# Optimization experiments

Measured on AMD Instinct MI355X. Metric: run time of the kernel, lower is better.

Reference implementation:

```python
import jax, jax.numpy as jnp
import numpy as np

VOCAB, EMB_DIM, HIDDEN, NUM_CLASSES = 100000, 128, 256, 20
B, S = 4096, 200


def setup_inputs() -> dict:
    key = jax.random.key(0)
    k1, k2, k3, k4, k5, k6, k7 = jax.random.split(key, 7)
    x = jax.random.randint(k1, (B, S), 0, VOCAB, dtype=jnp.int64)
    seq_lengths = jnp.maximum(jax.random.randint(k2, (B,), 0, S, dtype=jnp.int64), 1)
    emb = jax.random.normal(k3, (VOCAB, EMB_DIM), dtype=jnp.float32) * 0.02
    emb = emb.at[0].set(0.0)  # padding_idx=0
    W1 = jax.random.normal(k4, (EMB_DIM, HIDDEN), dtype=jnp.float32) * (1.0 / np.sqrt(EMB_DIM))
    b1 = jax.random.normal(k5, (HIDDEN,), dtype=jnp.float32) * 0.01
    W2 = jax.random.normal(k6, (HIDDEN, NUM_CLASSES), dtype=jnp.float32) * (1.0 / np.sqrt(HIDDEN))
    b2 = jax.random.normal(k7, (NUM_CLASSES,), dtype=jnp.float32) * 0.01
    return {"x": x, "seq_lengths": seq_lengths, "emb": emb, "W1": W1, "b1": b1, "W2": W2, "b2": b2}


def reference(x, seq_lengths, emb, W1, b1, W2, b2):
    # Embedding lookup: [B, S, D]
    e = emb[x]
    # Masked mean over first seq_lengths[i] positions (fused, no per-sample loop)
    mask = (jnp.arange(S)[None, :] < seq_lengths[:, None]).astype(e.dtype)  # [B, S]
    pooled = jnp.einsum('bsd,bs->bd', e, mask) / seq_lengths[:, None].astype(e.dtype)
    # MLP (dropout is identity in eval mode)
    hidden = jax.nn.relu(pooled @ W1 + b1)
    return hidden @ W2 + b2
```

## Files before the change

### kernel.cpp

```cpp
#include <hip/hip_runtime.h>
#include <hip/hip_bf16.h>

#define B 4096
#define S 200
#define EMB_DIM 128
#define HIDDEN 256
#define NUM_CLASSES 20
#define VOCAB 100000
#define NSLICE 8
#define SDIM 16
#define SP 224

typedef __attribute__((ext_vector_type(8))) unsigned short ushort8;

__device__ __forceinline__ unsigned short f2bf(float f) {
    unsigned u = __float_as_uint(f);
    unsigned r = u + 0x7fffu + ((u >> 16) & 1u);
    return (unsigned short)(r >> 16);
}

__global__ __launch_bounds__(256) void convert_kernel(
    const float* __restrict__ emb,
    unsigned short* __restrict__ embh)
{
    const int t = threadIdx.x;
    const int v = blockIdx.x * 16 + (t >> 4);
    const int d = t & 15;
    const float4 a = *(const float4*)(emb + (long)v * EMB_DIM + d * 8);
    const float4 b = *(const float4*)(emb + (long)v * EMB_DIM + d * 8 + 4);
    ushort8 o;
    o[0] = f2bf(a.x); o[1] = f2bf(a.y); o[2] = f2bf(a.z); o[3] = f2bf(a.w);
    o[4] = f2bf(b.x); o[5] = f2bf(b.y); o[6] = f2bf(b.z); o[7] = f2bf(b.w);
    const int s = d >> 1, h = d & 1;
    *(ushort8*)(embh + (long)s * VOCAB * SDIM + (long)v * SDIM + h * 8) = o;
}

__global__ __launch_bounds__(256) void gather_kernel(
    const int* __restrict__ x,
    const int* __restrict__ lens,
    const unsigned short* __restrict__ embh,
    float* __restrict__ pooled)
{
    __shared__ int sidx[8][SP];
    __shared__ int sL[8];

    const int t  = threadIdx.x;
    const int s  = blockIdx.x & 7;
    const int rg = blockIdx.x >> 3;
    const unsigned short* embS = embh + (long)s * VOCAB * SDIM;

    {
        const int r   = t >> 5;
        const int p0  = t & 31;
        const int row = rg * 8 + r;
        const int L   = lens[row];
        if (p0 == 0) sL[r] = L;
        for (int p = p0; p < SP; p += 32)
            sidx[r][p] = (p < L) ? x[(long)row * S + p] : 0;
    }
    __syncthreads();

    const int w  = t >> 6;
    const int l  = t & 63;
    const int pl = l >> 1;
    const int h  = l & 1;

    #pragma unroll
    for (int rr = 0; rr < 2; ++rr) {
        const int r2 = 2 * w + rr;
        const int L2 = sL[r2];
        const int nR = (L2 + 31) >> 5;

        float acc[8];
        #pragma unroll
        for (int f = 0; f < 8; ++f) acc[f] = 0.f;

        int cur = sidx[r2][pl];
        for (int it = 0; it < nR; ++it) {
            const uint4 q = *(const uint4*)(embS + (long)cur * SDIM + h * 8);
            const int nxt = (it + 1 < nR) ? sidx[r2][pl + ((it + 1) << 5)] : 0;
            acc[0] += __uint_as_float(q.x << 16);
            acc[1] += __uint_as_float(q.x & 0xffff0000u);
            acc[2] += __uint_as_float(q.y << 16);
            acc[3] += __uint_as_float(q.y & 0xffff0000u);
            acc[4] += __uint_as_float(q.z << 16);
            acc[5] += __uint_as_float(q.z & 0xffff0000u);
            acc[6] += __uint_as_float(q.w << 16);
            acc[7] += __uint_as_float(q.w & 0xffff0000u);
            cur = nxt;
        }

        #pragma unroll
        for (int st = 2; st <= 32; st <<= 1) {
            #pragma unroll
            for (int f = 0; f < 8; ++f) acc[f] += __shfl_xor(acc[f], st, 64);
        }

        if (l < 2) {
            const float invL = 1.0f / (float)L2;
            float* dst = pooled + (long)(rg * 8 + r2) * EMB_DIM + s * SDIM + h * 8;
            *(float4*)dst       = make_float4(acc[0] * invL, acc[1] * invL,
                                              acc[2] * invL, acc[3] * invL);
            *(float4*)(dst + 4) = make_float4(acc[4] * invL, acc[5] * invL,
                                              acc[6] * invL, acc[7] * invL);
        }
    }
}

#define TB 8
__global__ __launch_bounds__(256) void mlp_kernel(
    const float* __restrict__ pooled,
    const float* __restrict__ W1,
    const float* __restrict__ b1,
    const float* __restrict__ W2,
    const float* __restrict__ b2,
    float* __restrict__ out)
{
    __shared__ float P[TB][EMB_DIM];
    __shared__ float H[TB][HIDDEN];

    const int t = threadIdx.x;
    const int b0 = blockIdx.x * TB;

    for (int i = t; i < TB * EMB_DIM; i += 256)
        P[i >> 7][i & 127] = pooled[(long)b0 * EMB_DIM + i];
    __syncthreads();

    float acc[TB];
    #pragma unroll
    for (int r = 0; r < TB; ++r) acc[r] = 0.f;

    for (int k4 = 0; k4 < EMB_DIM; k4 += 4) {
        float4 p[TB];
        #pragma unroll
        for (int r = 0; r < TB; ++r) p[r] = *(const float4*)&P[r][k4];
        #pragma unroll
        for (int kk = 0; kk < 4; ++kk) {
            const float w = W1[(k4 + kk) * HIDDEN + t];
            #pragma unroll
            for (int r = 0; r < TB; ++r) {
                const float pv = (kk == 0) ? p[r].x : (kk == 1) ? p[r].y
                               : (kk == 2) ? p[r].z : p[r].w;
                acc[r] += pv * w;
            }
        }
    }

    const float bb = b1[t];
    #pragma unroll
    for (int r = 0; r < TB; ++r) H[r][t] = fmaxf(acc[r] + bb, 0.f);
    __syncthreads();

    if (t < TB * NUM_CLASSES) {
        const int r = t / NUM_CLASSES;
        const int c = t - r * NUM_CLASSES;
        float a0 = 0.f, a1 = 0.f;
        for (int k = 0; k < HIDDEN; k += 2) {
            a0 += H[r][k]     * W2[(k)     * NUM_CLASSES + c];
            a1 += H[r][k + 1] * W2[(k + 1) * NUM_CLASSES + c];
        }
        out[(long)(b0 + r) * NUM_CLASSES + c] = a0 + a1 + b2[c];
    }
}

extern "C" void kernel_launch(void* const* d_in, const int* in_sizes, int n_in,
                              void* d_out, int out_size, void* d_ws, size_t ws_size,
                              hipStream_t stream) {
    const int*   x    = (const int*)d_in[0];
    const int*   lens = (const int*)d_in[1];
    const float* emb  = (const float*)d_in[2];
    const float* W1   = (const float*)d_in[3];
    const float* b1   = (const float*)d_in[4];
    const float* W2   = (const float*)d_in[5];
    const float* b2   = (const float*)d_in[6];
    float*       out  = (float*)d_out;

    unsigned short* embh  = (unsigned short*)d_ws;
    float* pooled = (float*)((char*)d_ws + (long)VOCAB * EMB_DIM * 2);

    convert_kernel<<<VOCAB / 16, 256, 0, stream>>>(emb, embh);
    gather_kernel<<<(B / 8) * NSLICE, 256, 0, stream>>>(x, lens, embh, pooled);
    mlp_kernel<<<B / TB, 256, 0, stream>>>(pooled, W1, b1, W2, b2, out);
}
```

Before: 137.5 us.

## Partition gather by vocabulary range with per-slice partial sums

Splits the embedding-bag gather across blocks by vocabulary range instead of by embedding-dimension slice. Each block keeps a compacted shared-memory list of the tokens that fall in its vocab slice and reads full contiguous 256-byte bf16 rows. It writes per-slice partial means, which the MLP kernel then sums. The bf16 table reverts to a plain row-major layout. The aim is to keep each block's working set to one vocab slice of the table while getting contiguous row reads. The cost is an 8x larger intermediate buffer written and re-read, shared-memory atomics, padding of each list to a multiple of 16, and uneven per-slice token counts.

```diff
diff --git a/kernel.cpp b/kernel.cpp
--- a/kernel.cpp
+++ b/kernel.cpp
@@ -8,8 +8,9 @@
 #define NUM_CLASSES 20
 #define VOCAB 100000
 #define NSLICE 8
-#define SDIM 16
-#define SP 224
+#define VSLICE (VOCAB / NSLICE)
+#define RPB 8
+#define LCAP 208
 
 typedef __attribute__((ext_vector_type(8))) unsigned short ushort8;
 
@@ -23,82 +24,107 @@
     const float* __restrict__ emb,
     unsigned short* __restrict__ embh)
 {
-    const int t = threadIdx.x;
-    const int v = blockIdx.x * 16 + (t >> 4);
-    const int d = t & 15;
-    const float4 a = *(const float4*)(emb + (long)v * EMB_DIM + d * 8);
-    const float4 b = *(const float4*)(emb + (long)v * EMB_DIM + d * 8 + 4);
+    const long i = ((long)blockIdx.x * 256 + threadIdx.x) * 8;
+    const float4 a = *(const float4*)(emb + i);
+    const float4 b = *(const float4*)(emb + i + 4);
     ushort8 o;
     o[0] = f2bf(a.x); o[1] = f2bf(a.y); o[2] = f2bf(a.z); o[3] = f2bf(a.w);
     o[4] = f2bf(b.x); o[5] = f2bf(b.y); o[6] = f2bf(b.z); o[7] = f2bf(b.w);
-    const int s = d >> 1, h = d & 1;
-    *(ushort8*)(embh + (long)s * VOCAB * SDIM + (long)v * SDIM + h * 8) = o;
+    *(ushort8*)(embh + i) = o;
 }
 
 __global__ __launch_bounds__(256) void gather_kernel(
     const int* __restrict__ x,
     const int* __restrict__ lens,
     const unsigned short* __restrict__ embh,
-    float* __restrict__ pooled)
+    float* __restrict__ partial)
 {
-    __shared__ int sidx[8][SP];
-    __shared__ int sL[8];
-
-    const int t  = threadIdx.x;
-    const int s  = blockIdx.x & 7;
-    const int rg = blockIdx.x >> 3;
-    const unsigned short* embS = embh + (long)s * VOCAB * SDIM;
+    __shared__ int list[RPB][LCAP];
+    __shared__ int cnt[RPB];
+    __shared__ int pcnt[RPB];
+    __shared__ int sL[RPB];
+
+    const int t     = threadIdx.x;
+    const int slice = blockIdx.x & 7;
+    const int rg    = blockIdx.x >> 3;
+    const int vlo   = slice * VSLICE;
+
+    if (t < RPB) { cnt[t] = 0; sL[t] = lens[rg * RPB + t]; }
+    __syncthreads();
 
     {
         const int r   = t >> 5;
-        const int p0  = t & 31;
-        const int row = rg * 8 + r;
-        const int L   = lens[row];
-        if (p0 == 0) sL[r] = L;
-        for (int p = p0; p < SP; p += 32)
-            sidx[r][p] = (p < L) ? x[(long)row * S + p] : 0;
-    }
-    __syncthreads();
-
-    const int w  = t >> 6;
-    const int l  = t & 63;
-    const int pl = l >> 1;
-    const int h  = l & 1;
+        const int q   = t & 31;
+        const int row = rg * RPB + r;
+        const int L   = sL[r];
+        #pragma unroll
+        for (int j = 0; j < 7; ++j) {
+            const int p = q + 32 * j;
+            if (p < L) {
+                const int v = x[(long)row * S + p];
+                if ((unsigned)(v - vlo) < (unsigned)VSLICE) {
+                    const int pos = atomicAdd(&cnt[r], 1);
+                    if (pos < LCAP) list[r][pos] = v;
+                }
+            }
+        }
+    }
+    __syncthreads();
+
+    if (t < RPB) {
+        const int c  = cnt[t];
+        const int cp = (c + 15) & ~15;
+        for (int i = c; i < cp; ++i) list[t][i] = 0;
+        pcnt[t] = cp;
+    }
+    __syncthreads();
+
+    const int w = t >> 6;
+    const int l = t & 63;
+    const int g = l >> 4;
+    const int d = l & 15;
 
     #pragma unroll
     for (int rr = 0; rr < 2; ++rr) {
         const int r2 = 2 * w + rr;
-        const int L2 = sL[r2];
-        const int nR = (L2 + 31) >> 5;
+        const int n  = pcnt[r2];
 
         float acc[8];
         #pragma unroll
         for (int f = 0; f < 8; ++f) acc[f] = 0.f;
 
-        int cur = sidx[r2][pl];
-        for (int it = 0; it < nR; ++it) {
-            const uint4 q = *(const uint4*)(embS + (long)cur * SDIM + h * 8);
-            const int nxt = (it + 1 < nR) ? sidx[r2][pl + ((it + 1) << 5)] : 0;
-            acc[0] += __uint_as_float(q.x << 16);
-            acc[1] += __uint_as_float(q.x & 0xffff0000u);
-            acc[2] += __uint_as_float(q.y << 16);
-            acc[3] += __uint_as_float(q.y & 0xffff0000u);
-            acc[4] += __uint_as_float(q.z << 16);
-            acc[5] += __uint_as_float(q.z & 0xffff0000u);
-            acc[6] += __uint_as_float(q.w << 16);
-            acc[7] += __uint_as_float(q.w & 0xffff0000u);
-            cur = nxt;
-        }
-
-        #pragma unroll
-        for (int st = 2; st <= 32; st <<= 1) {
+        for (int base = 0; base < n; base += 16) {
+            const int i0 = list[r2][base + g];
+            const int i1 = list[r2][base + 4 + g];
+            const int i2 = list[r2][base + 8 + g];
+            const int i3 = list[r2][base + 12 + g];
+            const uint4 q0 = *(const uint4*)(embh + (long)i0 * EMB_DIM + d * 8);
+            const uint4 q1 = *(const uint4*)(embh + (long)i1 * EMB_DIM + d * 8);
+            const uint4 q2 = *(const uint4*)(embh + (long)i2 * EMB_DIM + d * 8);
+            const uint4 q3 = *(const uint4*)(embh + (long)i3 * EMB_DIM + d * 8);
             #pragma unroll
-            for (int f = 0; f < 8; ++f) acc[f] += __shfl_xor(acc[f], st, 64);
-        }
-
-        if (l < 2) {
-            const float invL = 1.0f / (float)L2;
-            float* dst = pooled + (long)(rg * 8 + r2) * EMB_DIM + s * SDIM + h * 8;
+            for (int k = 0; k < 4; ++k) {
+                const uint4 q = (k == 0) ? q0 : (k == 1) ? q1 : (k == 2) ? q2 : q3;
+                acc[0] += __uint_as_float(q.x << 16);
+                acc[1] += __uint_as_float(q.x & 0xffff0000u);
+                acc[2] += __uint_as_float(q.y << 16);
+                acc[3] += __uint_as_float(q.y & 0xffff0000u);
+                acc[4] += __uint_as_float(q.z << 16);
+                acc[5] += __uint_as_float(q.z & 0xffff0000u);
+                acc[6] += __uint_as_float(q.w << 16);
+                acc[7] += __uint_as_float(q.w & 0xffff0000u);
+            }
+        }
+
+        #pragma unroll
+        for (int f = 0; f < 8; ++f) {
+            acc[f] += __shfl_xor(acc[f], 16, 64);
+            acc[f] += __shfl_xor(acc[f], 32, 64);
+        }
+
+        if (l < 16) {
+            const float invL = 1.0f / (float)sL[r2];
+            float* dst = partial + ((long)slice * B + (rg * RPB + r2)) * EMB_DIM + l * 8;
             *(float4*)dst       = make_float4(acc[0] * invL, acc[1] * invL,
                                               acc[2] * invL, acc[3] * invL);
             *(float4*)(dst + 4) = make_float4(acc[4] * invL, acc[5] * invL,
@@ -109,7 +135,7 @@
 
 #define TB 8
 __global__ __launch_bounds__(256) void mlp_kernel(
-    const float* __restrict__ pooled,
+    const float* __restrict__ partial,
     const float* __restrict__ W1,
     const float* __restrict__ b1,
     const float* __restrict__ W2,
@@ -122,8 +148,13 @@
     const int t = threadIdx.x;
     const int b0 = blockIdx.x * TB;
 
-    for (int i = t; i < TB * EMB_DIM; i += 256)
-        P[i >> 7][i & 127] = pooled[(long)b0 * EMB_DIM + i];
+    for (int i = t; i < TB * EMB_DIM; i += 256) {
+        float s = 0.f;
+        #pragma unroll
+        for (int k = 0; k < NSLICE; ++k)
+            s += partial[(long)k * B * EMB_DIM + (long)b0 * EMB_DIM + i];
+        P[i >> 7][i & 127] = s;
+    }
     __syncthreads();
 
     float acc[TB];
@@ -136,12 +167,12 @@
         for (int r = 0; r < TB; ++r) p[r] = *(const float4*)&P[r][k4];
         #pragma unroll
         for (int kk = 0; kk < 4; ++kk) {
-            const float w = W1[(k4 + kk) * HIDDEN + t];
+            const float wv = W1[(k4 + kk) * HIDDEN + t];
             #pragma unroll
             for (int r = 0; r < TB; ++r) {
                 const float pv = (kk == 0) ? p[r].x : (kk == 1) ? p[r].y
                                : (kk == 2) ? p[r].z : p[r].w;
-                acc[r] += pv * w;
+                acc[r] += pv * wv;
             }
         }
     }
@@ -175,10 +206,10 @@
     const float* b2   = (const float*)d_in[6];
     float*       out  = (float*)d_out;
 
-    unsigned short* embh  = (unsigned short*)d_ws;
-    float* pooled = (float*)((char*)d_ws + (long)VOCAB * EMB_DIM * 2);
-
-    convert_kernel<<<VOCAB / 16, 256, 0, stream>>>(emb, embh);
-    gather_kernel<<<(B / 8) * NSLICE, 256, 0, stream>>>(x, lens, embh, pooled);
-    mlp_kernel<<<B / TB, 256, 0, stream>>>(pooled, W1, b1, W2, b2, out);
-}
+    unsigned short* embh = (unsigned short*)d_ws;
+    float* partial = (float*)((char*)d_ws + (long)VOCAB * EMB_DIM * 2);
+
+    convert_kernel<<<(VOCAB * EMB_DIM) / (8 * 256), 256, 0, stream>>>(emb, embh);
+    gather_kernel<<<(B / RPB) * NSLICE, 256, 0, stream>>>(x, lens, embh, partial);
+    mlp_kernel<<<B / TB, 256, 0, stream>>>(partial, W1, b1, W2, b2, out);
+}
```

New measurement: 134.9 us. Within noise of the previous version (-1.9%).
